# Kernel optimization log

Hardware: AMD Instinct MI355X
Metric: run time of the kernel (lower is better)

The kernel has to match this reference:

```python
import jax, jax.numpy as jnp
import numpy as np

B, T, C, H = 256, 256, 64, 512


def _uni(key, shape, stdv):
    return jax.random.uniform(key, shape, minval=-stdv, maxval=stdv, dtype=jnp.float32)


def setup_inputs() -> dict:
    key = jax.random.key(0)
    ks = jax.random.split(key, 16)
    data = jax.random.normal(ks[0], (B, T, C), dtype=jnp.float32)
    nan_mask = jax.random.uniform(ks[1], (B, T, C)) < 0.2
    data = jnp.where(nan_mask, jnp.nan, data)
    s_lstm = 1.0 / np.sqrt(H)
    s_c = 1.0 / np.sqrt(C)
    s_h = 1.0 / np.sqrt(H)
    return {
        'data': data,
        # LSTMCell (input = 2*C), PyTorch gate order i,f,g,o
        'W_ih': _uni(ks[2], (4 * H, 2 * C), s_lstm),
        'W_hh': _uni(ks[3], (4 * H, H), s_lstm),
        'b_ih': _uni(ks[4], (4 * H,), s_lstm),
        'b_hh': _uni(ks[5], (4 * H,), s_lstm),
        # temp_decay_h: TemporalDecay(C -> H), stdv = 1/sqrt(W.size(0)) = 1/sqrt(H)
        'W_gh': _uni(ks[6], (H, C), s_h),
        'b_gh': _uni(ks[7], (H,), s_h),
        # temp_decay_x: diag TemporalDecay(C -> C)
        'W_gx': _uni(ks[8], (C, C), s_c),
        'b_gx': _uni(ks[9], (C,), s_c),
        # hist_reg: Linear(H -> C)
        'W_hist': _uni(ks[10], (C, H), s_h),
        'b_hist': _uni(ks[11], (C,), s_h),
        'W_feat': _uni(ks[12], (C, C), s_c),
        'b_feat': _uni(ks[13], (C,), s_c),
        # weight_combine: Linear(2C -> C)
        'W_comb': _uni(ks[14], (C, 2 * C), 1.0 / np.sqrt(2 * C)),
        'b_comb': _uni(ks[15], (C,), 1.0 / np.sqrt(2 * C)),
    }


def delta_calc(masks):
    # masks: [B, T, C]. delta[:,0]=0; delta[:,1]=1; for t>=2:
    # decay = 1 if mask[:,t-1]==1 else decay+1, delta[:,t]=decay.
    b, t, c = masks.shape
    m_prev = jnp.moveaxis(masks[:, 1:t - 1, :], 1, 0)  # [T-2, B, C]

    def step(decay, mp):
        nd = jnp.where(mp == 1.0, 1.0, decay + 1.0)
        return nd, nd

    _, ds = jax.lax.scan(step, jnp.ones((b, c), masks.dtype), m_prev)
    return jnp.concatenate(
        [jnp.zeros((b, 1, c), masks.dtype),
         jnp.ones((b, 1, c), masks.dtype),
         jnp.moveaxis(ds, 0, 1)], axis=1)


def reference(data, W_ih, W_hh, b_ih, b_hh, W_gh, b_gh, W_gx, b_gx,
              W_hist, b_hist, W_feat, b_feat, W_comb, b_comb):
    masks = (~jnp.isnan(data)).astype(data.dtype)
    values = jnp.nan_to_num(data)
    deltas = delta_calc(masks)
    c_dim = data.shape[-1]
    eye = jnp.eye(c_dim, dtype=data.dtype)
    W_gx_m = W_gx * eye            # diag TemporalDecay mask
    W_feat_m = W_feat * (1.0 - eye)

    xs = (jnp.moveaxis(values, 1, 0), jnp.moveaxis(masks, 1, 0),
          jnp.moveaxis(deltas, 1, 0))  # time-major [T,B,C]

    def step(carry, tmd):
        h, c = carry
        x, m, d = tmd
        gamma_h = jnp.exp(-jax.nn.relu(d @ W_gh.T + b_gh))
        gamma_x = jnp.exp(-jax.nn.relu(d @ W_gx_m.T + b_gx))
        h = h * gamma_h
        x_h = h @ W_hist.T + b_hist
        x_c = m * x + (1.0 - m) * x_h
        z_h = x_c @ W_feat_m.T + b_feat
        alpha = jnp.concatenate([gamma_x, m], axis=1) @ W_comb.T + b_comb
        c_h = alpha * z_h + (1.0 - alpha) * x_h
        c_c = m * x + (1.0 - m) * c_h
        inp = jnp.concatenate([c_c, m], axis=1)
        gates = inp @ W_ih.T + b_ih + h @ W_hh.T + b_hh
        gi, gf, gg, go = jnp.split(gates, 4, axis=1)
        c_new = jax.nn.sigmoid(gf) * c + jax.nn.sigmoid(gi) * jnp.tanh(gg)
        h_new = jax.nn.sigmoid(go) * jnp.tanh(c_new)
        return (h_new, c_new), c_c

    hb = data.shape[0]
    hd = W_hh.shape[1]
    init = (jnp.zeros((hb, hd), data.dtype), jnp.zeros((hb, hd), data.dtype))
    _, imps = jax.lax.scan(step, init, xs)
    return jnp.moveaxis(imps, 0, 1)  # [B, T, C]
```

## Files before the change

### kernel.cpp

```cpp
#include <hip/hip_runtime.h>

typedef unsigned short ushort_t;
typedef unsigned int uint_t;
typedef unsigned long long ull_t;
typedef short v8s __attribute__((ext_vector_type(8)));
typedef float v4f __attribute__((ext_vector_type(4)));

__device__ __forceinline__ float b2f(ushort_t u) {
    uint_t x = ((uint_t)u) << 16;
    float f;
    __builtin_memcpy(&f, &x, 4);
    return f;
}
__device__ __forceinline__ ushort_t f2b(float f) {
    uint_t x;
    __builtin_memcpy(&x, &f, 4);
    uint_t r = (x + 0x7FFFu + ((x >> 16) & 1u)) >> 16;
    return (ushort_t)r;
}

__global__ __launch_bounds__(256) void k_setup(
    const float* __restrict__ Wih, const float* __restrict__ Whh,
    const float* __restrict__ Wgh, const float* __restrict__ Whist,
    const float* __restrict__ Wfeat,
    ushort_t* __restrict__ Wih_b, ushort_t* __restrict__ Whh_b,
    ushort_t* __restrict__ Wgh_b, ushort_t* __restrict__ Whist_b,
    ushort_t* __restrict__ Wfeat_b, ull_t* __restrict__ hbufs) {
    int bid = blockIdx.x, tid = threadIdx.x;
    if (bid < 64) {
        ull_t* p = hbufs + (size_t)bid * 4096 + tid;
#pragma unroll
        for (int i = 0; i < 16; ++i) p[i * 256] = 0;
        return;
    }
    bid -= 64;
    const float* src; ushort_t* dst; int n;
    if (bid < 1024)      { src = Wih;   dst = Wih_b;   n = 262144; }
    else if (bid < 5120) { bid -= 1024; src = Whh;   dst = Whh_b;   n = 1048576; }
    else if (bid < 5248) { bid -= 5120; src = Wgh;   dst = Wgh_b;   n = 32768; }
    else if (bid < 5376) { bid -= 5248; src = Whist; dst = Whist_b; n = 32768; }
    else                 { bid -= 5376; src = Wfeat; dst = Wfeat_b; n = 4096; }
    int i = bid * 256 + tid;
    if (i < n) dst[i] = f2b(src[i]);
}

__global__ __launch_bounds__(256) void k_pre(
    const float* __restrict__ data, const float* __restrict__ Wgx,
    const float* __restrict__ bgx,
    ushort_t* __restrict__ values, ushort_t* __restrict__ masks,
    ushort_t* __restrict__ deltas, ushort_t* __restrict__ gammax) {
    __shared__ int lastl[32][9];
    int tid = threadIdx.x;
    int j = tid >> 5, p = tid & 31;
    int pid = blockIdx.x * 32 + p;
    int b = pid >> 6, c = pid & 63;
    float wd = Wgx[c * 64 + c], bg = bgx[c];
    int t0 = j * 32;
    const float* dp = data + (size_t)b * 16384 + c;
    float v[32]; uint_t bits = 0;
#pragma unroll
    for (int s = 0; s < 32; ++s) {
        float x = dp[(t0 + s) * 64];
        bool obs = (x == x);
        v[s] = obs ? x : 0.f;
        bits |= obs ? (1u << s) : 0u;
    }
    uint_t vb = bits;
    if (j == 0) vb &= ~1u;
    int lastloc = 0;
    if (vb) lastloc = t0 + (31 - __clz(vb));
    lastl[p][j] = lastloc;
    __syncthreads();
    int L = 0;
    for (int jj = 0; jj < j; ++jj) L = max(L, lastl[p][jj]);
#pragma unroll
    for (int s = 0; s < 32; ++s) {
        int t = t0 + s;
        float m = ((bits >> s) & 1) ? 1.f : 0.f;
        float d = (t == 0) ? 0.f : (float)(t - L);
        float sg = d * wd + bg;
        float gx = (sg > 0.f) ? __expf(-sg) : 1.f;
        size_t o = (size_t)t * 16384 + pid;
        values[o] = f2b(v[s]); masks[o] = f2b(m);
        deltas[o] = f2b(d);    gammax[o] = f2b(gx);
        if (((bits >> s) & 1) && t >= 1) L = t;
    }
}

__global__ __launch_bounds__(256) void k_alpha(
    const ushort_t* __restrict__ gammax, const ushort_t* __restrict__ masks,
    const float* __restrict__ Wcomb, const float* __restrict__ bcomb,
    ushort_t* __restrict__ alpha) {
    __shared__ __attribute__((aligned(16))) ushort_t wl[64 * 136];
    __shared__ __attribute__((aligned(16))) ushort_t al[16 * 136];
    int tid = threadIdx.x;
    for (int idx = tid; idx < 8192; idx += 256) {
        int r = idx >> 7, kcol = idx & 127;
        wl[r * 136 + kcol] = f2b(Wcomb[idx]);
    }
    int tb0 = blockIdx.x * 16;
    for (int idx = tid; idx < 2048; idx += 256) {
        int r = idx >> 7, kcol = idx & 127;
        al[r * 136 + kcol] = (kcol < 64)
            ? gammax[(size_t)(tb0 + r) * 64 + kcol]
            : masks[(size_t)(tb0 + r) * 64 + (kcol - 64)];
    }
    __syncthreads();
    int i = tid & 63, rg = (tid >> 6) * 4;
    float bc = bcomb[i];
    float acc[4] = {bc, bc, bc, bc};
#pragma unroll
    for (int k8 = 0; k8 < 16; ++k8) {
        v8s w8 = *(const v8s*)(wl + i * 136 + k8 * 8);
#pragma unroll
        for (int rr = 0; rr < 4; ++rr) {
            v8s a8 = *(const v8s*)(al + (rg + rr) * 136 + k8 * 8);
#pragma unroll
            for (int q = 0; q < 8; ++q)
                acc[rr] += b2f((ushort_t)a8[q]) * b2f((ushort_t)w8[q]);
        }
    }
#pragma unroll
    for (int rr = 0; rr < 4; ++rr)
        alpha[(size_t)(tb0 + rg + rr) * 64 + i] = f2b(acc[rr]);
}

__global__ __launch_bounds__(256, 1) void k_run(
    const ushort_t* __restrict__ values, const ushort_t* __restrict__ masks,
    const ushort_t* __restrict__ deltas, const ushort_t* __restrict__ alpha,
    const ushort_t* __restrict__ Wih, const ushort_t* __restrict__ Whh,
    const float* __restrict__ bih, const float* __restrict__ bhh,
    const ushort_t* __restrict__ Wgh, const float* __restrict__ bgh,
    const ushort_t* __restrict__ Whist, const float* __restrict__ bhist,
    const ushort_t* __restrict__ Wfeat, const float* __restrict__ bfeat,
    ushort_t* __restrict__ hbufs, float* __restrict__ out) {
    __shared__ __attribute__((aligned(16))) ushort_t hlds[16 * 520];
    __shared__ __attribute__((aligned(16))) ushort_t inplds[16 * 136];
    __shared__ __attribute__((aligned(16))) ushort_t xclds[16 * 72];
    __shared__ __attribute__((aligned(16))) ushort_t d1b[16 * 72];
    __shared__ __attribute__((aligned(16))) float gl[4 * 16 * 36];
    __shared__ __attribute__((aligned(16))) float gam[16 * 36];

    int tid = threadIdx.x;
    int w = tid >> 6;
    int lane = tid & 63;
    int l15 = lane & 15, quad = lane >> 4;
    int wg = blockIdx.x;
    int rb = wg & 15, cb = wg >> 4;
    int b0 = rb * 16;

    v8s whhF[2][16], wihF[2][4], whisF[16], wfF[2], wghF[2] = {};
    float biasv[2];
#pragma unroll
    for (int nt2 = 0; nt2 < 2; ++nt2) {
        int hc = cb * 32 + nt2 * 16 + l15;
        int rW = w * 512 + hc;
        const ushort_t* whrow = Whh + (size_t)rW * 512;
        const ushort_t* wirow = Wih + (size_t)rW * 128;
#pragma unroll
        for (int kt = 0; kt < 16; ++kt)
            whhF[nt2][kt] = *(const v8s*)(whrow + kt * 32 + quad * 8);
#pragma unroll
        for (int kt = 0; kt < 4; ++kt)
            wihF[nt2][kt] = *(const v8s*)(wirow + kt * 32 + quad * 8);
        biasv[nt2] = bih[rW] + bhh[rW];
    }
    int colC = w * 16 + l15;
    {
        const ushort_t* hrow = Whist + (size_t)colC * 512;
#pragma unroll
        for (int kt = 0; kt < 16; ++kt)
            whisF[kt] = *(const v8s*)(hrow + kt * 32 + quad * 8);
        const ushort_t* frow = Wfeat + colC * 64;
#pragma unroll
        for (int kt = 0; kt < 2; ++kt) {
            int k0 = kt * 32 + quad * 8;
            v8s bb = *(const v8s*)(frow + k0);
#pragma unroll
            for (int j = 0; j < 8; ++j)
                if (k0 + j == colC) bb[j] = 0;
            wfF[kt] = bb;
        }
    }
    float bghv = 0.f;
    if (w < 2) {
        int gcol = cb * 32 + w * 16 + l15;
        const ushort_t* grow = Wgh + gcol * 64;
#pragma unroll
        for (int kt = 0; kt < 2; ++kt)
            wghF[kt] = *(const v8s*)(grow + kt * 32 + quad * 8);
        bghv = bgh[gcol];
    }
    float bhistv = bhist[colC];
    float bfeatv = bfeat[colC];

    int sf_row = tid >> 3, sf_c4 = (tid & 7) * 4;
    float c_reg4[4] = {0.f, 0.f, 0.f, 0.f};

    for (int t = 0; t < 256; ++t) {
        float v4r[4], m4r[4], a4r[4];
#pragma unroll
        for (int r = 0; r < 4; ++r) {
            int row = quad * 4 + r;
            size_t g = (size_t)t * 16384 + (b0 + row) * 64 + colC;
            v4r[r] = b2f(values[g]);
            m4r[r] = b2f(masks[g]);
            a4r[r] = b2f(alpha[g]);
        }
        v8s mreg = {}, dreg = {};
        if (tid < 128) {
            int row = tid >> 3, c8 = (tid & 7) * 8;
            int tn = (t < 255) ? t + 1 : 255;
            mreg = *(const v8s*)(masks + (size_t)t * 16384 + (b0 + row) * 64 + c8);
            dreg = *(const v8s*)(deltas + (size_t)tn * 16384 + (b0 + row) * 64 + c8);
        }

        if (t == 0) {
            v8s z = {0, 0, 0, 0, 0, 0, 0, 0};
            for (int idx = tid; idx < 1040; idx += 256) ((v8s*)hlds)[idx] = z;
        } else {
            const ushort_t* hb = hbufs + (size_t)(t & 7) * 131072;
            const ull_t* hp[8];
            ull_t hv[8];
#pragma unroll
            for (int i = 0; i < 8; ++i) {
                int c = tid + 256 * i;
                int row = c >> 7, c4 = (c & 127) * 4;
                hp[i] = (const ull_t*)(hb + (b0 + row) * 512 + c4);
                hv[i] = __hip_atomic_load(hp[i], __ATOMIC_RELAXED,
                                          __HIP_MEMORY_SCOPE_AGENT);
            }
            int guard = 0;
            while (true) {
                bool any = false;
#pragma unroll
                for (int i = 0; i < 8; ++i) any |= (hv[i] == 0);
                if (!any || ++guard > (1 << 20)) break;
                __builtin_amdgcn_s_sleep(1);
#pragma unroll
                for (int i = 0; i < 8; ++i)
                    if (hv[i] == 0)
                        hv[i] = __hip_atomic_load(hp[i], __ATOMIC_RELAXED,
                                                  __HIP_MEMORY_SCOPE_AGENT);
            }
#pragma unroll
            for (int i = 0; i < 8; ++i) {
                int c = tid + 256 * i;
                int row = c >> 7, c4 = (c & 127) * 4;
                *(ull_t*)(hlds + row * 520 + c4) =
                    hv[i] - 0x0001000100010001ULL;
            }
        }
        if (tid < 128) {
            int row = tid >> 3, c8 = (tid & 7) * 8;
            *(v8s*)(inplds + row * 136 + 64 + c8) = mreg;
            *(v8s*)(d1b + row * 72 + c8) = dreg;
        }
        __syncthreads();

        v4f accx = {0.f, 0.f, 0.f, 0.f};
        v4f accg0 = {0.f, 0.f, 0.f, 0.f}, accg1 = {0.f, 0.f, 0.f, 0.f};
#pragma unroll
        for (int kt = 0; kt < 16; ++kt) {
            v8s a = *(const v8s*)(hlds + l15 * 520 + kt * 32 + quad * 8);
            accx = __builtin_amdgcn_mfma_f32_16x16x32_bf16(a, whisF[kt], accx, 0, 0, 0);
            accg0 = __builtin_amdgcn_mfma_f32_16x16x32_bf16(a, whhF[0][kt], accg0, 0, 0, 0);
            accg1 = __builtin_amdgcn_mfma_f32_16x16x32_bf16(a, whhF[1][kt], accg1, 0, 0, 0);
        }
        if (w < 2) {
            v4f acc = {0.f, 0.f, 0.f, 0.f};
#pragma unroll
            for (int kt = 0; kt < 2; ++kt) {
                v8s a = *(const v8s*)(d1b + l15 * 72 + kt * 32 + quad * 8);
                acc = __builtin_amdgcn_mfma_f32_16x16x32_bf16(a, wghF[kt], acc, 0, 0, 0);
            }
#pragma unroll
            for (int r = 0; r < 4; ++r) {
                float s = acc[r] + bghv;
                gam[(quad * 4 + r) * 36 + w * 16 + l15] = (s > 0.f) ? __expf(-s) : 1.f;
            }
        }
        float xh4[4];
#pragma unroll
        for (int r = 0; r < 4; ++r) {
            float xh = accx[r] + bhistv;
            float xc = m4r[r] * v4r[r] + (1.f - m4r[r]) * xh;
            xclds[(quad * 4 + r) * 72 + colC] = f2b(xc);
            xh4[r] = xh;
        }
        __syncthreads();

        {
            v4f accz = {0.f, 0.f, 0.f, 0.f};
#pragma unroll
            for (int kt = 0; kt < 2; ++kt) {
                v8s a = *(const v8s*)(xclds + l15 * 72 + kt * 32 + quad * 8);
                accz = __builtin_amdgcn_mfma_f32_16x16x32_bf16(a, wfF[kt], accz, 0, 0, 0);
            }
#pragma unroll
            for (int r = 0; r < 4; ++r) {
                float zh = accz[r] + bfeatv;
                float ch = a4r[r] * zh + (1.f - a4r[r]) * xh4[r];
                float cc = m4r[r] * v4r[r] + (1.f - m4r[r]) * ch;
                int row = quad * 4 + r;
                inplds[row * 136 + colC] = f2b(cc);
                if (cb == 0)
                    out[(size_t)(b0 + row) * 16384 + t * 64 + colC] = cc;
            }
        }
        __syncthreads();

#pragma unroll
        for (int nt2 = 0; nt2 < 2; ++nt2) {
            v4f acc = (nt2 == 0) ? accg0 : accg1;
#pragma unroll
            for (int kt = 0; kt < 4; ++kt) {
                v8s a = *(const v8s*)(inplds + l15 * 136 + kt * 32 + quad * 8);
                acc = __builtin_amdgcn_mfma_f32_16x16x32_bf16(a, wihF[nt2][kt], acc, 0, 0, 0);
            }
#pragma unroll
            for (int r = 0; r < 4; ++r)
                gl[w * 576 + (quad * 4 + r) * 36 + nt2 * 16 + l15] = acc[r] + biasv[nt2];
        }
        __syncthreads();

        if (tid < 128) {
            ull_t outv = 0;
#pragma unroll
            for (int j = 0; j < 4; ++j) {
                int hcl = sf_c4 + j;
                float gi = gl[0 * 576 + sf_row * 36 + hcl];
                float gf = gl[1 * 576 + sf_row * 36 + hcl];
                float gg = gl[2 * 576 + sf_row * 36 + hcl];
                float go = gl[3 * 576 + sf_row * 36 + hcl];
                float si = 1.f / (1.f + __expf(-gi));
                float sf = 1.f / (1.f + __expf(-gf));
                float tg = 1.f - 2.f / (__expf(2.f * gg) + 1.f);
                float so = 1.f / (1.f + __expf(-go));
                float cn = sf * c_reg4[j] + si * tg;
                c_reg4[j] = cn;
                float hn = so * (1.f - 2.f / (__expf(2.f * cn) + 1.f));
                float g = gam[sf_row * 36 + hcl];
                outv |= (ull_t)(ushort_t)(f2b(hn * g) + 1) << (16 * j);
            }
            size_t myoff = (size_t)(b0 + sf_row) * 512 + cb * 32 + sf_c4;
            if (t < 255) {
                ushort_t* hnx = hbufs + (size_t)((t + 1) & 7) * 131072;
                __hip_atomic_store((ull_t*)(hnx + myoff), outv,
                                   __ATOMIC_RELAXED, __HIP_MEMORY_SCOPE_AGENT);
            }
            if (t + 4 < 256) {
                ushort_t* hz = hbufs + (size_t)((t + 4) & 7) * 131072;
                __hip_atomic_store((ull_t*)(hz + myoff), 0ULL,
                                   __ATOMIC_RELAXED, __HIP_MEMORY_SCOPE_AGENT);
            }
        }
        __syncthreads();
    }
}

extern "C" void kernel_launch(void* const* d_in, const int* in_sizes, int n_in,
                              void* d_out, int out_size, void* d_ws, size_t ws_size,
                              hipStream_t stream) {
    const float* data  = (const float*)d_in[0];
    const float* Wih   = (const float*)d_in[1];
    const float* Whh   = (const float*)d_in[2];
    const float* bih   = (const float*)d_in[3];
    const float* bhh   = (const float*)d_in[4];
    const float* Wgh   = (const float*)d_in[5];
    const float* bgh   = (const float*)d_in[6];
    const float* Wgx   = (const float*)d_in[7];
    const float* bgx   = (const float*)d_in[8];
    const float* Whist = (const float*)d_in[9];
    const float* bhist = (const float*)d_in[10];
    const float* Wfeat = (const float*)d_in[11];
    const float* bfeat = (const float*)d_in[12];
    const float* Wcomb = (const float*)d_in[13];
    const float* bcomb = (const float*)d_in[14];
    float* out = (float*)d_out;

    char* ws = (char*)d_ws;
    const size_t NTBC = 256UL * 256 * 64;
    ushort_t* valuesb = (ushort_t*)ws; ws += NTBC * 2;
    ushort_t* masksp  = (ushort_t*)ws; ws += NTBC * 2;
    ushort_t* deltasp = (ushort_t*)ws; ws += NTBC * 2;
    ushort_t* gammax  = (ushort_t*)ws; ws += NTBC * 2;
    ushort_t* alphap  = (ushort_t*)ws; ws += NTBC * 2;
    ushort_t* Wih_b   = (ushort_t*)ws; ws += 2048UL * 128 * 2;
    ushort_t* Whh_b   = (ushort_t*)ws; ws += 2048UL * 512 * 2;
    ushort_t* Wgh_b   = (ushort_t*)ws; ws += 512UL * 64 * 2;
    ushort_t* Whist_b = (ushort_t*)ws; ws += 64UL * 512 * 2;
    ushort_t* Wfeat_b = (ushort_t*)ws; ws += 64UL * 64 * 2;
    ushort_t* hbufs   = (ushort_t*)ws; ws += 8UL * 131072 * 2;

    k_setup<<<5456, 256, 0, stream>>>(Wih, Whh, Wgh, Whist, Wfeat,
                                      Wih_b, Whh_b, Wgh_b, Whist_b, Wfeat_b,
                                      (ull_t*)hbufs);
    k_pre<<<512, 256, 0, stream>>>(data, Wgx, bgx, valuesb, masksp, deltasp, gammax);
    k_alpha<<<4096, 256, 0, stream>>>(gammax, masksp, Wcomb, bcomb, alphap);
    k_run<<<256, 256, 0, stream>>>(valuesb, masksp, deltasp, alphap,
                                   Wih_b, Whh_b, bih, bhh,
                                   Wgh_b, bgh, Whist_b, bhist,
                                   Wfeat_b, bfeat, hbufs, out);
}
```

Baseline: 967.0 us.

## Use inline-asm sc0 loads/stores for cross-block hidden-state exchange polling

Replaces the per-element relaxed atomic loads of the shared hidden-state buffer with a batched inline-asm block of eight global_load_dwordx2 sc0 loads and a single waitcnt. The polling loop now alternates these batched loads with occasional atomic loads. The zeroing of the future ring slot moves earlier, into the input-load phase, and each hidden-state store is issued twice, once as an sc0 asm store and once as an atomic store. The output write is spread across blocks (row == cb) instead of being done only by cb==0. The aim is lower latency for the cross-workgroup h handoff, at the risk of memory-coherence subtleties, since sc0 may not guarantee agent-scope visibility, and the early zeroing is now done by threads tid<128 using sf_row-based offsets, which may not cover the same slots.

```diff
diff --git a/kernel.cpp b/kernel.cpp
--- a/kernel.cpp
+++ b/kernel.cpp
@@ -17,6 +17,32 @@
     __builtin_memcpy(&x, &f, 4);
     uint_t r = (x + 0x7FFFu + ((x >> 16) & 1u)) >> 16;
     return (ushort_t)r;
+}
+
+__device__ __forceinline__ void fast_load8(const ull_t* p0, const ull_t* p1,
+                                           const ull_t* p2, const ull_t* p3,
+                                           const ull_t* p4, const ull_t* p5,
+                                           const ull_t* p6, const ull_t* p7,
+                                           ull_t* v) {
+    asm volatile(
+        "global_load_dwordx2 %0, %8, off sc0\n\t"
+        "global_load_dwordx2 %1, %9, off sc0\n\t"
+        "global_load_dwordx2 %2, %10, off sc0\n\t"
+        "global_load_dwordx2 %3, %11, off sc0\n\t"
+        "global_load_dwordx2 %4, %12, off sc0\n\t"
+        "global_load_dwordx2 %5, %13, off sc0\n\t"
+        "global_load_dwordx2 %6, %14, off sc0\n\t"
+        "global_load_dwordx2 %7, %15, off sc0\n\t"
+        "s_waitcnt vmcnt(0)"
+        : "=&v"(v[0]), "=&v"(v[1]), "=&v"(v[2]), "=&v"(v[3]),
+          "=&v"(v[4]), "=&v"(v[5]), "=&v"(v[6]), "=&v"(v[7])
+        : "v"(p0), "v"(p1), "v"(p2), "v"(p3),
+          "v"(p4), "v"(p5), "v"(p6), "v"(p7)
+        : "memory");
+}
+__device__ __forceinline__ void fast_store(ull_t* p, ull_t v) {
+    asm volatile("global_store_dwordx2 %0, %1, off sc0"
+                 :: "v"(p), "v"(v) : "memory");
 }
 
 __global__ __launch_bounds__(256) void k_setup(
@@ -195,6 +221,7 @@
     float bfeatv = bfeat[colC];
 
     int sf_row = tid >> 3, sf_c4 = (tid & 7) * 4;
+    size_t myoff = (size_t)(b0 + sf_row) * 512 + cb * 32 + sf_c4;
     float c_reg4[4] = {0.f, 0.f, 0.f, 0.f};
 
     for (int t = 0; t < 256; ++t) {
@@ -213,6 +240,12 @@
             int tn = (t < 255) ? t + 1 : 255;
             mreg = *(const v8s*)(masks + (size_t)t * 16384 + (b0 + row) * 64 + c8);
             dreg = *(const v8s*)(deltas + (size_t)tn * 16384 + (b0 + row) * 64 + c8);
+            if (t + 4 < 256) {
+                ull_t* zp = (ull_t*)(hbufs + (size_t)((t + 4) & 7) * 131072 + myoff);
+                fast_store(zp, 0ULL);
+                __hip_atomic_store(zp, 0ULL, __ATOMIC_RELAXED,
+                                   __HIP_MEMORY_SCOPE_AGENT);
+            }
         }
 
         if (t == 0) {
@@ -226,10 +259,9 @@
             for (int i = 0; i < 8; ++i) {
                 int c = tid + 256 * i;
                 int row = c >> 7, c4 = (c & 127) * 4;
-                hp[i] = (const ull_t*)(hb + (b0 + row) * 512 + c4);
-                hv[i] = __hip_atomic_load(hp[i], __ATOMIC_RELAXED,
-                                          __HIP_MEMORY_SCOPE_AGENT);
-            }
+                hp[i] = (const ull_t*)(hb + (size_t)(b0 + row) * 512 + c4);
+            }
+            fast_load8(hp[0], hp[1], hp[2], hp[3], hp[4], hp[5], hp[6], hp[7], hv);
             int guard = 0;
             while (true) {
                 bool any = false;
@@ -237,11 +269,20 @@
                 for (int i = 0; i < 8; ++i) any |= (hv[i] == 0);
                 if (!any || ++guard > (1 << 20)) break;
                 __builtin_amdgcn_s_sleep(1);
-#pragma unroll
-                for (int i = 0; i < 8; ++i)
-                    if (hv[i] == 0)
-                        hv[i] = __hip_atomic_load(hp[i], __ATOMIC_RELAXED,
-                                                  __HIP_MEMORY_SCOPE_AGENT);
+                if ((guard & 3) == 3) {
+#pragma unroll
+                    for (int i = 0; i < 8; ++i)
+                        if (hv[i] == 0)
+                            hv[i] = __hip_atomic_load(hp[i], __ATOMIC_RELAXED,
+                                                      __HIP_MEMORY_SCOPE_AGENT);
+                } else {
+                    ull_t tv[8];
+                    fast_load8(hp[0], hp[1], hp[2], hp[3],
+                               hp[4], hp[5], hp[6], hp[7], tv);
+#pragma unroll
+                    for (int i = 0; i < 8; ++i)
+                        if (hv[i] == 0) hv[i] = tv[i];
+                }
             }
 #pragma unroll
             for (int i = 0; i < 8; ++i) {
@@ -304,7 +345,7 @@
                 float cc = m4r[r] * v4r[r] + (1.f - m4r[r]) * ch;
                 int row = quad * 4 + r;
                 inplds[row * 136 + colC] = f2b(cc);
-                if (cb == 0)
+                if (row == cb)
                     out[(size_t)(b0 + row) * 16384 + t * 64 + colC] = cc;
             }
         }
@@ -343,16 +384,11 @@
                 float g = gam[sf_row * 36 + hcl];
                 outv |= (ull_t)(ushort_t)(f2b(hn * g) + 1) << (16 * j);
             }
-            size_t myoff = (size_t)(b0 + sf_row) * 512 + cb * 32 + sf_c4;
             if (t < 255) {
-                ushort_t* hnx = hbufs + (size_t)((t + 1) & 7) * 131072;
-                __hip_atomic_store((ull_t*)(hnx + myoff), outv,
-                                   __ATOMIC_RELAXED, __HIP_MEMORY_SCOPE_AGENT);
-            }
-            if (t + 4 < 256) {
-                ushort_t* hz = hbufs + (size_t)((t + 4) & 7) * 131072;
-                __hip_atomic_store((ull_t*)(hz + myoff), 0ULL,
-                                   __ATOMIC_RELAXED, __HIP_MEMORY_SCOPE_AGENT);
+                ull_t* sp = (ull_t*)(hbufs + (size_t)((t + 1) & 7) * 131072 + myoff);
+                fast_store(sp, outv);
+                __hip_atomic_store(sp, outv, __ATOMIC_RELAXED,
+                                   __HIP_MEMORY_SCOPE_AGENT);
             }
         }
         __syncthreads();
```

Measured after the change: 1.757 ms. 81.7% more time.

## Halve recurrent-kernel workgroups by giving each block 64 hidden columns

Applied to the files above, without the earlier changes.

The persistent LSTM kernel now launches 128 workgroups instead of 256. Each one owns 64 hidden columns per gate rather than 32, so it keeps four W_hh/W_ih fragment sets in registers and runs four gate MFMA chains per K step. All 256 threads now do the cell update, and zeroing of future h buffers moves to the top of the step. Output writes are spread across column blocks by row. This cuts the number of workgroups polling and exchanging h through global memory each step, and the redundant per-block hist/feat work. In exchange each block does twice the gate compute and uses far more registers, which may spill.

```diff
diff --git a/kernel.cpp b/kernel.cpp
--- a/kernel.cpp
+++ b/kernel.cpp
@@ -138,8 +138,8 @@
     __shared__ __attribute__((aligned(16))) ushort_t inplds[16 * 136];
     __shared__ __attribute__((aligned(16))) ushort_t xclds[16 * 72];
     __shared__ __attribute__((aligned(16))) ushort_t d1b[16 * 72];
-    __shared__ __attribute__((aligned(16))) float gl[4 * 16 * 36];
-    __shared__ __attribute__((aligned(16))) float gam[16 * 36];
+    __shared__ __attribute__((aligned(16))) float gl[4 * 16 * 68];
+    __shared__ __attribute__((aligned(16))) float gam[16 * 68];
 
     int tid = threadIdx.x;
     int w = tid >> 6;
@@ -149,11 +149,11 @@
     int rb = wg & 15, cb = wg >> 4;
     int b0 = rb * 16;
 
-    v8s whhF[2][16], wihF[2][4], whisF[16], wfF[2], wghF[2] = {};
-    float biasv[2];
-#pragma unroll
-    for (int nt2 = 0; nt2 < 2; ++nt2) {
-        int hc = cb * 32 + nt2 * 16 + l15;
+    v8s whhF[4][16], wihF[4][4], whisF[16], wfF[2], wghF[2];
+    float biasv[4];
+#pragma unroll
+    for (int nt2 = 0; nt2 < 4; ++nt2) {
+        int hc = cb * 64 + nt2 * 16 + l15;
         int rW = w * 512 + hc;
         const ushort_t* whrow = Whh + (size_t)rW * 512;
         const ushort_t* wirow = Wih + (size_t)rW * 128;
@@ -182,9 +182,9 @@
             wfF[kt] = bb;
         }
     }
-    float bghv = 0.f;
-    if (w < 2) {
-        int gcol = cb * 32 + w * 16 + l15;
+    float bghv;
+    {
+        int gcol = cb * 64 + w * 16 + l15;
         const ushort_t* grow = Wgh + gcol * 64;
 #pragma unroll
         for (int kt = 0; kt < 2; ++kt)
@@ -194,7 +194,8 @@
     float bhistv = bhist[colC];
     float bfeatv = bfeat[colC];
 
-    int sf_row = tid >> 3, sf_c4 = (tid & 7) * 4;
+    int sf_row = tid >> 4, sf_c4 = (tid & 15) * 4;
+    size_t myoff = (size_t)(b0 + sf_row) * 512 + cb * 64 + sf_c4;
     float c_reg4[4] = {0.f, 0.f, 0.f, 0.f};
 
     for (int t = 0; t < 256; ++t) {
@@ -213,6 +214,11 @@
             int tn = (t < 255) ? t + 1 : 255;
             mreg = *(const v8s*)(masks + (size_t)t * 16384 + (b0 + row) * 64 + c8);
             dreg = *(const v8s*)(deltas + (size_t)tn * 16384 + (b0 + row) * 64 + c8);
+        }
+        if (t + 4 < 256) {
+            ull_t* zp = (ull_t*)(hbufs + (size_t)((t + 4) & 7) * 131072 + myoff);
+            __hip_atomic_store(zp, 0ULL, __ATOMIC_RELAXED,
+                               __HIP_MEMORY_SCOPE_AGENT);
         }
 
         if (t == 0) {
@@ -226,7 +232,7 @@
             for (int i = 0; i < 8; ++i) {
                 int c = tid + 256 * i;
                 int row = c >> 7, c4 = (c & 127) * 4;
-                hp[i] = (const ull_t*)(hb + (b0 + row) * 512 + c4);
+                hp[i] = (const ull_t*)(hb + (size_t)(b0 + row) * 512 + c4);
                 hv[i] = __hip_atomic_load(hp[i], __ATOMIC_RELAXED,
                                           __HIP_MEMORY_SCOPE_AGENT);
             }
@@ -259,15 +265,18 @@
         __syncthreads();
 
         v4f accx = {0.f, 0.f, 0.f, 0.f};
-        v4f accg0 = {0.f, 0.f, 0.f, 0.f}, accg1 = {0.f, 0.f, 0.f, 0.f};
+        v4f accg[4] = {{0.f, 0.f, 0.f, 0.f}, {0.f, 0.f, 0.f, 0.f},
+                       {0.f, 0.f, 0.f, 0.f}, {0.f, 0.f, 0.f, 0.f}};
 #pragma unroll
         for (int kt = 0; kt < 16; ++kt) {
             v8s a = *(const v8s*)(hlds + l15 * 520 + kt * 32 + quad * 8);
             accx = __builtin_amdgcn_mfma_f32_16x16x32_bf16(a, whisF[kt], accx, 0, 0, 0);
-            accg0 = __builtin_amdgcn_mfma_f32_16x16x32_bf16(a, whhF[0][kt], accg0, 0, 0, 0);
-            accg1 = __builtin_amdgcn_mfma_f32_16x16x32_bf16(a, whhF[1][kt], accg1, 0, 0, 0);
-        }
-        if (w < 2) {
+            accg[0] = __builtin_amdgcn_mfma_f32_16x16x32_bf16(a, whhF[0][kt], accg[0], 0, 0, 0);
+            accg[1] = __builtin_amdgcn_mfma_f32_16x16x32_bf16(a, whhF[1][kt], accg[1], 0, 0, 0);
+            accg[2] = __builtin_amdgcn_mfma_f32_16x16x32_bf16(a, whhF[2][kt], accg[2], 0, 0, 0);
+            accg[3] = __builtin_amdgcn_mfma_f32_16x16x32_bf16(a, whhF[3][kt], accg[3], 0, 0, 0);
+        }
+        {
             v4f acc = {0.f, 0.f, 0.f, 0.f};
 #pragma unroll
             for (int kt = 0; kt < 2; ++kt) {
@@ -277,7 +286,7 @@
 #pragma unroll
             for (int r = 0; r < 4; ++r) {
                 float s = acc[r] + bghv;
-                gam[(quad * 4 + r) * 36 + w * 16 + l15] = (s > 0.f) ? __expf(-s) : 1.f;
+                gam[(quad * 4 + r) * 68 + w * 16 + l15] = (s > 0.f) ? __expf(-s) : 1.f;
             }
         }
         float xh4[4];
@@ -304,15 +313,15 @@
                 float cc = m4r[r] * v4r[r] + (1.f - m4r[r]) * ch;
                 int row = quad * 4 + r;
                 inplds[row * 136 + colC] = f2b(cc);
-                if (cb == 0)
+                if ((row >> 1) == cb)
                     out[(size_t)(b0 + row) * 16384 + t * 64 + colC] = cc;
             }
         }
         __syncthreads();
 
 #pragma unroll
-        for (int nt2 = 0; nt2 < 2; ++nt2) {
-            v4f acc = (nt2 == 0) ? accg0 : accg1;
+        for (int nt2 = 0; nt2 < 4; ++nt2) {
+            v4f acc = accg[nt2];
 #pragma unroll
             for (int kt = 0; kt < 4; ++kt) {
                 v8s a = *(const v8s*)(inplds + l15 * 136 + kt * 32 + quad * 8);
@@ -320,19 +329,19 @@
             }
 #pragma unroll
             for (int r = 0; r < 4; ++r)
-                gl[w * 576 + (quad * 4 + r) * 36 + nt2 * 16 + l15] = acc[r] + biasv[nt2];
+                gl[w * 1088 + (quad * 4 + r) * 68 + nt2 * 16 + l15] = acc[r] + biasv[nt2];
         }
         __syncthreads();
 
-        if (tid < 128) {
+        {
             ull_t outv = 0;
 #pragma unroll
             for (int j = 0; j < 4; ++j) {
                 int hcl = sf_c4 + j;
-                float gi = gl[0 * 576 + sf_row * 36 + hcl];
-                float gf = gl[1 * 576 + sf_row * 36 + hcl];
-                float gg = gl[2 * 576 + sf_row * 36 + hcl];
-                float go = gl[3 * 576 + sf_row * 36 + hcl];
+                float gi = gl[0 * 1088 + sf_row * 68 + hcl];
+                float gf = gl[1 * 1088 + sf_row * 68 + hcl];
+                float gg = gl[2 * 1088 + sf_row * 68 + hcl];
+                float go = gl[3 * 1088 + sf_row * 68 + hcl];
                 float si = 1.f / (1.f + __expf(-gi));
                 float sf = 1.f / (1.f + __expf(-gf));
                 float tg = 1.f - 2.f / (__expf(2.f * gg) + 1.f);
@@ -340,19 +349,13 @@
                 float cn = sf * c_reg4[j] + si * tg;
                 c_reg4[j] = cn;
                 float hn = so * (1.f - 2.f / (__expf(2.f * cn) + 1.f));
-                float g = gam[sf_row * 36 + hcl];
+                float g = gam[sf_row * 68 + hcl];
                 outv |= (ull_t)(ushort_t)(f2b(hn * g) + 1) << (16 * j);
             }
-            size_t myoff = (size_t)(b0 + sf_row) * 512 + cb * 32 + sf_c4;
             if (t < 255) {
-                ushort_t* hnx = hbufs + (size_t)((t + 1) & 7) * 131072;
-                __hip_atomic_store((ull_t*)(hnx + myoff), outv,
-                                   __ATOMIC_RELAXED, __HIP_MEMORY_SCOPE_AGENT);
-            }
-            if (t + 4 < 256) {
-                ushort_t* hz = hbufs + (size_t)((t + 4) & 7) * 131072;
-                __hip_atomic_store((ull_t*)(hz + myoff), 0ULL,
-                                   __ATOMIC_RELAXED, __HIP_MEMORY_SCOPE_AGENT);
+                ull_t* sp = (ull_t*)(hbufs + (size_t)((t + 1) & 7) * 131072 + myoff);
+                __hip_atomic_store(sp, outv, __ATOMIC_RELAXED,
+                                   __HIP_MEMORY_SCOPE_AGENT);
             }
         }
         __syncthreads();
@@ -398,7 +401,7 @@
                                       (ull_t*)hbufs);
     k_pre<<<512, 256, 0, stream>>>(data, Wgx, bgx, valuesb, masksp, deltasp, gammax);
     k_alpha<<<4096, 256, 0, stream>>>(gammax, masksp, Wcomb, bcomb, alphap);
-    k_run<<<256, 256, 0, stream>>>(valuesb, masksp, deltasp, alphap,
+    k_run<<<128, 256, 0, stream>>>(valuesb, masksp, deltasp, alphap,
                                    Wih_b, Whh_b, bih, bhh,
                                    Wgh_b, bgh, Whist_b, bhist,
                                    Wfeat_b, bfeat, hbufs, out);
```

Result: slower. 1.520 ms (+57.2%).
